# Optimization experiments

Measured on AMD Instinct MI355X. Metric: run time of the kernel, lower is better.

The kernel has to match this reference:

```python
import jax, jax.numpy as jnp
import numpy as np

E, D, H, T = 8, 1024, 2048, 2048  # num_expert, d_model, d_hidden, tokens

def setup_inputs() -> dict:
    key = jax.random.key(0)
    ks = jax.random.split(key, 7)
    return {
        "moe_inp": jax.random.normal(ks[0], (T, D), jnp.float32),
        "Wg": jax.random.normal(ks[1], (D, E), jnp.float32) * 0.02,
        "bg": jnp.zeros((E,), jnp.float32),
        "W1": jax.random.normal(ks[2], (E, D, H), jnp.float32) * 0.02,
        "b1": jnp.zeros((E, H), jnp.float32),
        "W2": jax.random.normal(ks[3], (E, H, D), jnp.float32) * 0.02,
        "b2": jnp.zeros((E, D), jnp.float32),
        "top_k": 2,
    }

def reference(moe_inp, Wg, bg, W1, b1, W2, b2, top_k):
    # NaiveGate: linear gate, top-k select, softmax over the selected logits
    logits = moe_inp @ Wg + bg                      # [T, E]
    top_vals, top_idx = jax.lax.top_k(logits, top_k)  # [T, k]
    gate_score = jax.nn.softmax(top_vals, axis=-1)    # [T, k]

    # Exact (no capacity drop) MoE: scan over experts, mask-combine.
    # Equivalent math to scatter -> per-expert FFN -> gather -> bmm(gate_score, ...).
    def body(acc, xs):
        e, w1, bb1, w2, bb2 = xs
        h = jax.nn.gelu(moe_inp @ w1 + bb1)          # [T, H]
        y = h @ w2 + bb2                             # [T, D]
        w = jnp.sum(jnp.where(top_idx == e, gate_score, 0.0), axis=-1)  # [T]
        return acc + w[:, None] * y, None

    init = jnp.zeros_like(moe_inp)
    xs = (jnp.arange(E), W1, b1, W2, b2)
    moe_outp, _ = jax.lax.scan(body, init, xs)
    return moe_outp, top_idx
```

## Files before the change

kernel.cpp:

```cpp
#include <hip/hip_runtime.h>
#include <stdint.h>

#define T_TOK 2048
#define D_DIM 1024
#define H_DIM 2048
#define N_EXP 8
#define MAXS  4608

#define WS_CNT    0
#define WS_BTOK   256
#define WS_BW     (WS_BTOK + N_EXP*2048*4)
#define WS_XG     (WS_BW + N_EXP*2048*4)
#define WS_HBUF   (WS_XG + (size_t)MAXS*1024*2)
#define WS_W1T    (WS_HBUF + (size_t)MAXS*2048*2)
#define WS_W2T    (WS_W1T + (size_t)N_EXP*1024*2048*2)

typedef __bf16 bf16x8 __attribute__((ext_vector_type(8)));
typedef float  f32x4  __attribute__((ext_vector_type(4)));

__device__ __forceinline__ unsigned short f2bf(float f) {
  unsigned int u = __float_as_uint(f);
  u += 0x7fffu + ((u >> 16) & 1u);
  return (unsigned short)(u >> 16);
}

__device__ __forceinline__ float gelu_tanh(float x) {
  const float u = 0.7978845608028654f * (x + 0.044715f * x * x * x);
  const float t = __expf(-2.0f * fabsf(u));
  const float th = (1.0f - t) * __builtin_amdgcn_rcpf(1.0f + t);
  return 0.5f * x * (1.0f + copysignf(th, u));
}

__global__ void zero_kernel(float4* __restrict__ out4, int* __restrict__ cnt) {
  int i = blockIdx.x * 256 + threadIdx.x;
  out4[i] = make_float4(0.f, 0.f, 0.f, 0.f);
  if (blockIdx.x == 0 && threadIdx.x < N_EXP) cnt[threadIdx.x] = 0;
}

__global__ void gate_kernel(const float* __restrict__ x, const float* __restrict__ Wg,
                            const float* __restrict__ bg, float* __restrict__ out_idx,
                            int* __restrict__ cnt, int* __restrict__ btok,
                            float* __restrict__ bw) {
  const int lane = threadIdx.x & 63;
  const int t = blockIdx.x * 4 + (threadIdx.x >> 6);
  float p[8];
#pragma unroll
  for (int i = 0; i < 8; ++i) p[i] = 0.f;
  const float* xr = x + (size_t)t * D_DIM;
  for (int i = lane; i < D_DIM; i += 64) {
    const float xv = xr[i];
    const float4 wa = ((const float4*)(Wg + i * 8))[0];
    const float4 wb = ((const float4*)(Wg + i * 8))[1];
    p[0] += xv * wa.x; p[1] += xv * wa.y; p[2] += xv * wa.z; p[3] += xv * wa.w;
    p[4] += xv * wb.x; p[5] += xv * wb.y; p[6] += xv * wb.z; p[7] += xv * wb.w;
  }
#pragma unroll
  for (int off = 32; off > 0; off >>= 1) {
#pragma unroll
    for (int i = 0; i < 8; ++i) p[i] += __shfl_xor(p[i], off);
  }
  if (lane == 0) {
#pragma unroll
    for (int i = 0; i < 8; ++i) p[i] += bg[i];
    int i0 = 0; float v0 = p[0];
#pragma unroll
    for (int i = 1; i < 8; ++i) if (p[i] > v0) { v0 = p[i]; i0 = i; }
    int i1 = -1; float v1 = -3.4e38f;
#pragma unroll
    for (int i = 0; i < 8; ++i) if (i != i0 && p[i] > v1) { v1 = p[i]; i1 = i; }
    const float ex = expf(v1 - v0);
    const float inv = 1.f / (1.f + ex);
    out_idx[t * 2 + 0] = (float)i0;
    out_idx[t * 2 + 1] = (float)i1;
    int s0 = atomicAdd(&cnt[i0], 1);
    btok[i0 * 2048 + s0] = t; bw[i0 * 2048 + s0] = inv;
    int s1 = atomicAdd(&cnt[i1], 1);
    btok[i1 * 2048 + s1] = t; bw[i1 * 2048 + s1] = ex * inv;
  }
}

__global__ void transpose_cvt(const float* __restrict__ W1, unsigned short* __restrict__ W1t,
                              const float* __restrict__ W2, unsigned short* __restrict__ W2t) {
  const int set = blockIdx.z;
  const int e = blockIdx.y;
  const int lin = blockIdx.x;
  const int R = set ? H_DIM : D_DIM;
  const int C = set ? D_DIM : H_DIM;
  const int tx = set ? (lin & 15) : (lin & 31);
  const int ty = set ? (lin >> 4) : (lin >> 5);
  const float* in = (set ? W2 : W1) + (size_t)e * (D_DIM * H_DIM);
  unsigned short* out = (set ? W2t : W1t) + (size_t)e * (D_DIM * H_DIM);
  const int c0 = tx * 64, r0 = ty * 64;
  __shared__ float tile[64][68];
  const int tid = threadIdx.x;
#pragma unroll
  for (int p = 0; p < 4; ++p) {
    const int idx = p * 256 + tid;
    const int r = idx >> 4, c4 = idx & 15;
    *(float4*)&tile[r][c4 * 4] = *(const float4*)(in + (size_t)(r0 + r) * C + c0 + c4 * 4);
  }
  __syncthreads();
#pragma unroll
  for (int p = 0; p < 2; ++p) {
    const int idx = p * 256 + tid;
    const int oc = idx >> 3, seg = idx & 7;
    unsigned u[4];
#pragma unroll
    for (int j = 0; j < 4; ++j) {
      const unsigned lo = f2bf(tile[seg * 8 + 2 * j][oc]);
      const unsigned hi = f2bf(tile[seg * 8 + 2 * j + 1][oc]);
      u[j] = lo | (hi << 16);
    }
    *(uint4*)(out + (size_t)(c0 + oc) * R + r0 + seg * 8) = make_uint4(u[0], u[1], u[2], u[3]);
  }
}

__device__ __forceinline__ void expert_seg(const int* __restrict__ cnt, int e,
                                           int& base, int& ce, int& pcnt, int& total) {
  int off = 0; base = 0; ce = 0; pcnt = 0;
#pragma unroll
  for (int i = 0; i < N_EXP; ++i) {
    const int c = cnt[i];
    const int p = (c + 63) & ~63;
    if (i == e) { base = off; ce = c; pcnt = p; }
    off += p;
  }
  total = off;
}

__global__ void gather_cvt(const float* __restrict__ x, const int* __restrict__ cnt,
                           const int* __restrict__ btok, unsigned short* __restrict__ Xg) {
  const int s = blockIdx.x;
  int off = 0, e = -1, loc = 0, c_e = 0;
#pragma unroll
  for (int i = 0; i < N_EXP; ++i) {
    const int c = cnt[i];
    const int p = (c + 63) & ~63;
    if (e < 0 && s < off + p) { e = i; loc = s - off; c_e = c; }
    off += p;
  }
  if (e < 0) return;
  uint2* orow = (uint2*)(Xg + (size_t)s * D_DIM);
  if (loc < c_e) {
    const int t = btok[e * 2048 + loc];
    const float4 v = ((const float4*)(x + (size_t)t * D_DIM))[threadIdx.x];
    uint2 u;
    u.x = (unsigned)f2bf(v.x) | ((unsigned)f2bf(v.y) << 16);
    u.y = (unsigned)f2bf(v.z) | ((unsigned)f2bf(v.w) << 16);
    orow[threadIdx.x] = u;
  } else {
    orow[threadIdx.x] = make_uint2(0u, 0u);
  }
}

template <int MODE>
__global__ void __launch_bounds__(256) moe_gemm(
    const unsigned short* __restrict__ A, const unsigned short* __restrict__ B,
    const float* __restrict__ bias, const int* __restrict__ cnt,
    const int* __restrict__ btok, const float* __restrict__ bw,
    unsigned short* __restrict__ Hout, float* __restrict__ out) {
  constexpr int K   = (MODE == 0) ? D_DIM : H_DIM;
  constexpr int SK  = (MODE == 0) ? 1 : 2;
  constexpr int KS  = K / SK;
  constexpr int NIT = KS / 32;

  const int lin = blockIdx.x;
  const int glo = lin & 7;
  const int mt  = (lin >> 3) & 31;
  const int g   = ((lin >> 8) << 3) | glo;
  int nt, e, ksl;
  if (MODE == 0) { nt = g & 15; e = g >> 4; ksl = 0; }
  else           { nt = g & 7;  e = (g >> 3) & 7; ksl = g >> 6; }

  int base, ce, pcnt, total;
  expert_seg(cnt, e, base, ce, pcnt, total);
  if (mt * 64 >= pcnt) return;
  const int row0 = base + mt * 64;
  const int n0 = nt * 128;

  __shared__ __align__(16) unsigned short As[2][64 * 32];
  __shared__ __align__(16) unsigned short Bs[2][128 * 32];

  const int tid = threadIdx.x;
  const int lane = tid & 63;
  const int wv = tid >> 6;
  const int wm = wv >> 1;
  const int wn = wv & 1;

  const unsigned short* Ab = A + (size_t)row0 * K + ksl * KS;
  const unsigned short* Bb = B + (size_t)e * ((size_t)H_DIM * D_DIM) + (size_t)n0 * K + ksl * KS;

  f32x4 acc[2][4];
#pragma unroll
  for (int i = 0; i < 2; ++i)
#pragma unroll
    for (int j = 0; j < 4; ++j) acc[i][j] = (f32x4)(0.0f);

  const int subr = lane >> 2;
  const int ks = (lane & 3) * 8;
  const int fr = lane & 15;
  const int kq = (lane >> 4) * 8;

  auto stage = [&](int kt, int b) {
    const int k0 = kt * 32;
    {
      const int r = wv * 16 + subr;
      const unsigned short* ga = Ab + (size_t)r * K + (k0 + ks);
      __builtin_amdgcn_global_load_lds(
          (__attribute__((address_space(1))) void*)ga,
          (__attribute__((address_space(3))) void*)(As[b] + wv * 16 * 32), 16, 0, 0);
    }
#pragma unroll
    for (int it = 0; it < 2; ++it) {
      const int ci = wv + it * 4;
      const int r = ci * 16 + subr;
      const unsigned short* gb = Bb + (size_t)r * K + (k0 + ks);
      __builtin_amdgcn_global_load_lds(
          (__attribute__((address_space(1))) void*)gb,
          (__attribute__((address_space(3))) void*)(Bs[b] + ci * 16 * 32), 16, 0, 0);
    }
  };

  stage(0, 0);
  for (int i = 0; i < NIT; ++i) {
    const int b = i & 1;
    __syncthreads();
    if (i + 1 < NIT) stage(i + 1, b ^ 1);
    bf16x8 av[2], bv[4];
#pragma unroll
    for (int mi = 0; mi < 2; ++mi)
      av[mi] = *(const bf16x8*)(As[b] + (wm * 32 + mi * 16 + fr) * 32 + kq);
#pragma unroll
    for (int ni = 0; ni < 4; ++ni)
      bv[ni] = *(const bf16x8*)(Bs[b] + (wn * 64 + ni * 16 + fr) * 32 + kq);
#pragma unroll
    for (int mi = 0; mi < 2; ++mi)
#pragma unroll
      for (int ni = 0; ni < 4; ++ni)
        acc[mi][ni] = __builtin_amdgcn_mfma_f32_16x16x32_bf16(av[mi], bv[ni], acc[mi][ni], 0, 0, 0);
  }

  if (MODE == 0) {
    const float* bb = bias + (size_t)e * H_DIM + n0;
#pragma unroll
    for (int mi = 0; mi < 2; ++mi) {
      const int rb = wm * 32 + mi * 16 + (lane >> 4) * 4;
#pragma unroll
      for (int r = 0; r < 4; ++r) {
        unsigned short* hp = Hout + (size_t)(row0 + rb + r) * H_DIM + n0;
#pragma unroll
        for (int ni = 0; ni < 4; ++ni) {
          const int col = wn * 64 + ni * 16 + fr;
          hp[col] = f2bf(gelu_tanh(acc[mi][ni][r] + bb[col]));
        }
      }
    }
  } else {
    const float* bb = bias + (size_t)e * D_DIM + n0;
#pragma unroll
    for (int mi = 0; mi < 2; ++mi) {
      const int rb = wm * 32 + mi * 16 + (lane >> 4) * 4;
#pragma unroll
      for (int r = 0; r < 4; ++r) {
        const int local = mt * 64 + rb + r;
        if (local < ce) {
          const int tok = btok[e * 2048 + local];
          const float w = bw[e * 2048 + local];
          float* op = out + (size_t)tok * D_DIM + n0;
#pragma unroll
          for (int ni = 0; ni < 4; ++ni) {
            const int col = wn * 64 + ni * 16 + fr;
            const float bias_once = (ksl == 0) ? bb[col] : 0.f;
            atomicAdd(op + col, w * (acc[mi][ni][r] + bias_once));
          }
        }
      }
    }
  }
}

extern "C" void kernel_launch(void* const* d_in, const int* in_sizes, int n_in,
                              void* d_out, int out_size, void* d_ws, size_t ws_size,
                              hipStream_t stream) {
  const float* moe_inp = (const float*)d_in[0];
  const float* Wg = (const float*)d_in[1];
  const float* bg = (const float*)d_in[2];
  const float* W1 = (const float*)d_in[3];
  const float* b1 = (const float*)d_in[4];
  const float* W2 = (const float*)d_in[5];
  const float* b2 = (const float*)d_in[6];
  float* out = (float*)d_out;

  char* ws = (char*)d_ws;
  int* cnt  = (int*)(ws + WS_CNT);
  int* btok = (int*)(ws + WS_BTOK);
  float* bw = (float*)(ws + WS_BW);
  unsigned short* Xg   = (unsigned short*)(ws + WS_XG);
  unsigned short* Hbuf = (unsigned short*)(ws + WS_HBUF);
  unsigned short* W1t  = (unsigned short*)(ws + WS_W1T);
  unsigned short* W2t  = (unsigned short*)(ws + WS_W2T);

  zero_kernel<<<dim3(2048), dim3(256), 0, stream>>>((float4*)out, cnt);
  gate_kernel<<<dim3(T_TOK / 4), dim3(256), 0, stream>>>(moe_inp, Wg, bg,
                                                         out + (size_t)T_TOK * D_DIM,
                                                         cnt, btok, bw);
  transpose_cvt<<<dim3(512, N_EXP, 2), dim3(256), 0, stream>>>(W1, W1t, W2, W2t);
  gather_cvt<<<dim3(MAXS), dim3(256), 0, stream>>>(moe_inp, cnt, btok, Xg);
  moe_gemm<0><<<dim3(4096), dim3(256), 0, stream>>>(
      Xg, W1t, b1, cnt, btok, bw, Hbuf, nullptr);
  moe_gemm<1><<<dim3(4096), dim3(256), 0, stream>>>(
      Hbuf, W2t, b2, cnt, btok, bw, nullptr, out);
}
```

Measured before the change: 333.2 us.

## Merge prep kernels and overlap W2 transpose with first expert GEMM

Zeroing, gating and the W1 transpose now run in one prep kernel, with the expert counters cleared by a memset. The W2 transpose blocks are appended to the first GEMM's grid so its bandwidth-bound work can overlap the compute-bound GEMM. This cuts kernel launches and lets idle CUs take transpose work during the first GEMM's tail. The trade-off is larger shared-memory allocations in the fused kernels, which may lower occupancy, and more branching on block index.

Result: faster. 318.5 us (-4.4%).

```diff
diff --git a/kernel.cpp b/kernel.cpp
--- a/kernel.cpp
+++ b/kernel.cpp
@@ -31,18 +31,43 @@
   return 0.5f * x * (1.0f + copysignf(th, u));
 }
 
-__global__ void zero_kernel(float4* __restrict__ out4, int* __restrict__ cnt) {
-  int i = blockIdx.x * 256 + threadIdx.x;
-  out4[i] = make_float4(0.f, 0.f, 0.f, 0.f);
-  if (blockIdx.x == 0 && threadIdx.x < N_EXP) cnt[threadIdx.x] = 0;
-}
-
-__global__ void gate_kernel(const float* __restrict__ x, const float* __restrict__ Wg,
-                            const float* __restrict__ bg, float* __restrict__ out_idx,
-                            int* __restrict__ cnt, int* __restrict__ btok,
-                            float* __restrict__ bw) {
+
+__device__ __forceinline__ void transpose_body(const float* __restrict__ in,
+                                               unsigned short* __restrict__ out,
+                                               int Rout, int Cin, int tx, int ty,
+                                               void* smem_) {
+  float (*tile)[68] = (float (*)[68])smem_;
+  const int c0 = tx * 64, r0 = ty * 64;
+  const int tid = threadIdx.x;
+#pragma unroll
+  for (int p = 0; p < 4; ++p) {
+    const int idx = p * 256 + tid;
+    const int r = idx >> 4, c4 = idx & 15;
+    *(float4*)&tile[r][c4 * 4] = *(const float4*)(in + (size_t)(r0 + r) * Cin + c0 + c4 * 4);
+  }
+  __syncthreads();
+#pragma unroll
+  for (int p = 0; p < 2; ++p) {
+    const int idx = p * 256 + tid;
+    const int oc = idx >> 3, seg = idx & 7;
+    unsigned u[4];
+#pragma unroll
+    for (int j = 0; j < 4; ++j) {
+      const unsigned lo = f2bf(tile[seg * 8 + 2 * j][oc]);
+      const unsigned hi = f2bf(tile[seg * 8 + 2 * j + 1][oc]);
+      u[j] = lo | (hi << 16);
+    }
+    *(uint4*)(out + (size_t)(c0 + oc) * Rout + r0 + seg * 8) = make_uint4(u[0], u[1], u[2], u[3]);
+  }
+}
+
+__device__ __forceinline__ void gate_body(int t, const float* __restrict__ x,
+                                          const float* __restrict__ Wg,
+                                          const float* __restrict__ bg,
+                                          float* __restrict__ out_idx,
+                                          int* __restrict__ cnt, int* __restrict__ btok,
+                                          float* __restrict__ bw) {
   const int lane = threadIdx.x & 63;
-  const int t = blockIdx.x * 4 + (threadIdx.x >> 6);
   float p[8];
 #pragma unroll
   for (int i = 0; i < 8; ++i) p[i] = 0.f;
@@ -79,42 +104,6 @@
   }
 }
 
-__global__ void transpose_cvt(const float* __restrict__ W1, unsigned short* __restrict__ W1t,
-                              const float* __restrict__ W2, unsigned short* __restrict__ W2t) {
-  const int set = blockIdx.z;
-  const int e = blockIdx.y;
-  const int lin = blockIdx.x;
-  const int R = set ? H_DIM : D_DIM;
-  const int C = set ? D_DIM : H_DIM;
-  const int tx = set ? (lin & 15) : (lin & 31);
-  const int ty = set ? (lin >> 4) : (lin >> 5);
-  const float* in = (set ? W2 : W1) + (size_t)e * (D_DIM * H_DIM);
-  unsigned short* out = (set ? W2t : W1t) + (size_t)e * (D_DIM * H_DIM);
-  const int c0 = tx * 64, r0 = ty * 64;
-  __shared__ float tile[64][68];
-  const int tid = threadIdx.x;
-#pragma unroll
-  for (int p = 0; p < 4; ++p) {
-    const int idx = p * 256 + tid;
-    const int r = idx >> 4, c4 = idx & 15;
-    *(float4*)&tile[r][c4 * 4] = *(const float4*)(in + (size_t)(r0 + r) * C + c0 + c4 * 4);
-  }
-  __syncthreads();
-#pragma unroll
-  for (int p = 0; p < 2; ++p) {
-    const int idx = p * 256 + tid;
-    const int oc = idx >> 3, seg = idx & 7;
-    unsigned u[4];
-#pragma unroll
-    for (int j = 0; j < 4; ++j) {
-      const unsigned lo = f2bf(tile[seg * 8 + 2 * j][oc]);
-      const unsigned hi = f2bf(tile[seg * 8 + 2 * j + 1][oc]);
-      u[j] = lo | (hi << 16);
-    }
-    *(uint4*)(out + (size_t)(c0 + oc) * R + r0 + seg * 8) = make_uint4(u[0], u[1], u[2], u[3]);
-  }
-}
-
 __device__ __forceinline__ void expert_seg(const int* __restrict__ cnt, int e,
                                            int& base, int& ce, int& pcnt, int& total) {
   int off = 0; base = 0; ce = 0; pcnt = 0;
@@ -126,6 +115,152 @@
     off += p;
   }
   total = off;
+}
+
+template <int MODE>
+__device__ __forceinline__ void gemm_body(
+    int lin, const unsigned short* __restrict__ A, const unsigned short* __restrict__ B,
+    const float* __restrict__ bias, const int* __restrict__ cnt,
+    const int* __restrict__ btok, const float* __restrict__ bw,
+    unsigned short* __restrict__ Hout, float* __restrict__ out, void* smem_) {
+  constexpr int K   = (MODE == 0) ? D_DIM : H_DIM;
+  constexpr int SK  = (MODE == 0) ? 1 : 2;
+  constexpr int KS  = K / SK;
+  constexpr int NIT = KS / 32;
+
+  const int glo = lin & 7;
+  const int mt  = (lin >> 3) & 31;
+  const int g   = ((lin >> 8) << 3) | glo;
+  int nt, e, ksl;
+  if (MODE == 0) { nt = g & 15; e = g >> 4; ksl = 0; }
+  else           { nt = g & 7;  e = (g >> 3) & 7; ksl = g >> 6; }
+
+  int base, ce, pcnt, total;
+  expert_seg(cnt, e, base, ce, pcnt, total);
+  if (mt * 64 >= pcnt) return;
+  const int row0 = base + mt * 64;
+  const int n0 = nt * 128;
+
+  unsigned short (*As)[64 * 32] = (unsigned short (*)[64 * 32])smem_;
+  unsigned short (*Bs)[128 * 32] = (unsigned short (*)[128 * 32])((char*)smem_ + 8192);
+
+  const int tid = threadIdx.x;
+  const int lane = tid & 63;
+  const int wv = tid >> 6;
+  const int wm = wv >> 1;
+  const int wn = wv & 1;
+
+  const unsigned short* Ab = A + (size_t)row0 * K + ksl * KS;
+  const unsigned short* Bb = B + (size_t)e * ((size_t)H_DIM * D_DIM) + (size_t)n0 * K + ksl * KS;
+
+  f32x4 acc[2][4];
+#pragma unroll
+  for (int i = 0; i < 2; ++i)
+#pragma unroll
+    for (int j = 0; j < 4; ++j) acc[i][j] = (f32x4)(0.0f);
+
+  const int subr = lane >> 2;
+  const int ks = (lane & 3) * 8;
+  const int fr = lane & 15;
+  const int kq = (lane >> 4) * 8;
+
+  auto stage = [&](int kt, int b) {
+    const int k0 = kt * 32;
+    {
+      const int r = wv * 16 + subr;
+      const unsigned short* ga = Ab + (size_t)r * K + (k0 + ks);
+      __builtin_amdgcn_global_load_lds(
+          (__attribute__((address_space(1))) void*)ga,
+          (__attribute__((address_space(3))) void*)(As[b] + wv * 16 * 32), 16, 0, 0);
+    }
+#pragma unroll
+    for (int it = 0; it < 2; ++it) {
+      const int ci = wv + it * 4;
+      const int r = ci * 16 + subr;
+      const unsigned short* gb = Bb + (size_t)r * K + (k0 + ks);
+      __builtin_amdgcn_global_load_lds(
+          (__attribute__((address_space(1))) void*)gb,
+          (__attribute__((address_space(3))) void*)(Bs[b] + ci * 16 * 32), 16, 0, 0);
+    }
+  };
+
+  stage(0, 0);
+  for (int i = 0; i < NIT; ++i) {
+    const int b = i & 1;
+    __syncthreads();
+    if (i + 1 < NIT) stage(i + 1, b ^ 1);
+    bf16x8 av[2], bv[4];
+#pragma unroll
+    for (int mi = 0; mi < 2; ++mi)
+      av[mi] = *(const bf16x8*)(As[b] + (wm * 32 + mi * 16 + fr) * 32 + kq);
+#pragma unroll
+    for (int ni = 0; ni < 4; ++ni)
+      bv[ni] = *(const bf16x8*)(Bs[b] + (wn * 64 + ni * 16 + fr) * 32 + kq);
+#pragma unroll
+    for (int mi = 0; mi < 2; ++mi)
+#pragma unroll
+      for (int ni = 0; ni < 4; ++ni)
+        acc[mi][ni] = __builtin_amdgcn_mfma_f32_16x16x32_bf16(av[mi], bv[ni], acc[mi][ni], 0, 0, 0);
+  }
+
+  if (MODE == 0) {
+    const float* bb = bias + (size_t)e * H_DIM + n0;
+#pragma unroll
+    for (int mi = 0; mi < 2; ++mi) {
+      const int rb = wm * 32 + mi * 16 + (lane >> 4) * 4;
+#pragma unroll
+      for (int r = 0; r < 4; ++r) {
+        unsigned short* hp = Hout + (size_t)(row0 + rb + r) * H_DIM + n0;
+#pragma unroll
+        for (int ni = 0; ni < 4; ++ni) {
+          const int col = wn * 64 + ni * 16 + fr;
+          hp[col] = f2bf(gelu_tanh(acc[mi][ni][r] + bb[col]));
+        }
+      }
+    }
+  } else {
+    const float* bb = bias + (size_t)e * D_DIM + n0;
+#pragma unroll
+    for (int mi = 0; mi < 2; ++mi) {
+      const int rb = wm * 32 + mi * 16 + (lane >> 4) * 4;
+#pragma unroll
+      for (int r = 0; r < 4; ++r) {
+        const int local = mt * 64 + rb + r;
+        if (local < ce) {
+          const int tok = btok[e * 2048 + local];
+          const float w = bw[e * 2048 + local];
+          float* op = out + (size_t)tok * D_DIM + n0;
+#pragma unroll
+          for (int ni = 0; ni < 4; ++ni) {
+            const int col = wn * 64 + ni * 16 + fr;
+            const float bias_once = (ksl == 0) ? bb[col] : 0.f;
+            atomicAdd(op + col, w * (acc[mi][ni][r] + bias_once));
+          }
+        }
+      }
+    }
+  }
+}
+
+
+__global__ void __launch_bounds__(256) prep_kernel(
+    const float* __restrict__ x, const float* __restrict__ Wg,
+    const float* __restrict__ bg, const float* __restrict__ W1,
+    float* __restrict__ out, int* __restrict__ cnt, int* __restrict__ btok,
+    float* __restrict__ bw, unsigned short* __restrict__ W1t) {
+  __shared__ __align__(16) char smem[17408];
+  const int bid = blockIdx.x;
+  if (bid < 2048) {
+    ((float4*)out)[bid * 256 + threadIdx.x] = make_float4(0.f, 0.f, 0.f, 0.f);
+  } else if (bid < 2560) {
+    gate_body((bid - 2048) * 4 + (threadIdx.x >> 6), x, Wg, bg,
+              out + (size_t)T_TOK * D_DIM, cnt, btok, bw);
+  } else {
+    const int lin = bid - 2560;
+    const int e = lin >> 9, l9 = lin & 511;
+    transpose_body(W1 + (size_t)e * (D_DIM * H_DIM), W1t + (size_t)e * (D_DIM * H_DIM),
+                   D_DIM, H_DIM, l9 & 31, l9 >> 5, smem);
+  }
 }
 
 __global__ void gather_cvt(const float* __restrict__ x, const int* __restrict__ cnt,
@@ -153,130 +288,30 @@
   }
 }
 
-template <int MODE>
-__global__ void __launch_bounds__(256) moe_gemm(
-    const unsigned short* __restrict__ A, const unsigned short* __restrict__ B,
-    const float* __restrict__ bias, const int* __restrict__ cnt,
+__global__ void __launch_bounds__(256) gemm0_w2t(
+    const unsigned short* __restrict__ Xg, const unsigned short* __restrict__ W1t,
+    const float* __restrict__ b1, const int* __restrict__ cnt,
     const int* __restrict__ btok, const float* __restrict__ bw,
-    unsigned short* __restrict__ Hout, float* __restrict__ out) {
-  constexpr int K   = (MODE == 0) ? D_DIM : H_DIM;
-  constexpr int SK  = (MODE == 0) ? 1 : 2;
-  constexpr int KS  = K / SK;
-  constexpr int NIT = KS / 32;
-
-  const int lin = blockIdx.x;
-  const int glo = lin & 7;
-  const int mt  = (lin >> 3) & 31;
-  const int g   = ((lin >> 8) << 3) | glo;
-  int nt, e, ksl;
-  if (MODE == 0) { nt = g & 15; e = g >> 4; ksl = 0; }
-  else           { nt = g & 7;  e = (g >> 3) & 7; ksl = g >> 6; }
-
-  int base, ce, pcnt, total;
-  expert_seg(cnt, e, base, ce, pcnt, total);
-  if (mt * 64 >= pcnt) return;
-  const int row0 = base + mt * 64;
-  const int n0 = nt * 128;
-
-  __shared__ __align__(16) unsigned short As[2][64 * 32];
-  __shared__ __align__(16) unsigned short Bs[2][128 * 32];
-
-  const int tid = threadIdx.x;
-  const int lane = tid & 63;
-  const int wv = tid >> 6;
-  const int wm = wv >> 1;
-  const int wn = wv & 1;
-
-  const unsigned short* Ab = A + (size_t)row0 * K + ksl * KS;
-  const unsigned short* Bb = B + (size_t)e * ((size_t)H_DIM * D_DIM) + (size_t)n0 * K + ksl * KS;
-
-  f32x4 acc[2][4];
-#pragma unroll
-  for (int i = 0; i < 2; ++i)
-#pragma unroll
-    for (int j = 0; j < 4; ++j) acc[i][j] = (f32x4)(0.0f);
-
-  const int subr = lane >> 2;
-  const int ks = (lane & 3) * 8;
-  const int fr = lane & 15;
-  const int kq = (lane >> 4) * 8;
-
-  auto stage = [&](int kt, int b) {
-    const int k0 = kt * 32;
-    {
-      const int r = wv * 16 + subr;
-      const unsigned short* ga = Ab + (size_t)r * K + (k0 + ks);
-      __builtin_amdgcn_global_load_lds(
-          (__attribute__((address_space(1))) void*)ga,
-          (__attribute__((address_space(3))) void*)(As[b] + wv * 16 * 32), 16, 0, 0);
-    }
-#pragma unroll
-    for (int it = 0; it < 2; ++it) {
-      const int ci = wv + it * 4;
-      const int r = ci * 16 + subr;
-      const unsigned short* gb = Bb + (size_t)r * K + (k0 + ks);
-      __builtin_amdgcn_global_load_lds(
-          (__attribute__((address_space(1))) void*)gb,
-          (__attribute__((address_space(3))) void*)(Bs[b] + ci * 16 * 32), 16, 0, 0);
-    }
-  };
-
-  stage(0, 0);
-  for (int i = 0; i < NIT; ++i) {
-    const int b = i & 1;
-    __syncthreads();
-    if (i + 1 < NIT) stage(i + 1, b ^ 1);
-    bf16x8 av[2], bv[4];
-#pragma unroll
-    for (int mi = 0; mi < 2; ++mi)
-      av[mi] = *(const bf16x8*)(As[b] + (wm * 32 + mi * 16 + fr) * 32 + kq);
-#pragma unroll
-    for (int ni = 0; ni < 4; ++ni)
-      bv[ni] = *(const bf16x8*)(Bs[b] + (wn * 64 + ni * 16 + fr) * 32 + kq);
-#pragma unroll
-    for (int mi = 0; mi < 2; ++mi)
-#pragma unroll
-      for (int ni = 0; ni < 4; ++ni)
-        acc[mi][ni] = __builtin_amdgcn_mfma_f32_16x16x32_bf16(av[mi], bv[ni], acc[mi][ni], 0, 0, 0);
-  }
-
-  if (MODE == 0) {
-    const float* bb = bias + (size_t)e * H_DIM + n0;
-#pragma unroll
-    for (int mi = 0; mi < 2; ++mi) {
-      const int rb = wm * 32 + mi * 16 + (lane >> 4) * 4;
-#pragma unroll
-      for (int r = 0; r < 4; ++r) {
-        unsigned short* hp = Hout + (size_t)(row0 + rb + r) * H_DIM + n0;
-#pragma unroll
-        for (int ni = 0; ni < 4; ++ni) {
-          const int col = wn * 64 + ni * 16 + fr;
-          hp[col] = f2bf(gelu_tanh(acc[mi][ni][r] + bb[col]));
-        }
-      }
-    }
+    unsigned short* __restrict__ Hbuf, const float* __restrict__ W2,
+    unsigned short* __restrict__ W2t) {
+  __shared__ __align__(16) char smem[24576];
+  if (blockIdx.x < 4096) {
+    gemm_body<0>(blockIdx.x, Xg, W1t, b1, cnt, btok, bw, Hbuf, nullptr, smem);
   } else {
-    const float* bb = bias + (size_t)e * D_DIM + n0;
-#pragma unroll
-    for (int mi = 0; mi < 2; ++mi) {
-      const int rb = wm * 32 + mi * 16 + (lane >> 4) * 4;
-#pragma unroll
-      for (int r = 0; r < 4; ++r) {
-        const int local = mt * 64 + rb + r;
-        if (local < ce) {
-          const int tok = btok[e * 2048 + local];
-          const float w = bw[e * 2048 + local];
-          float* op = out + (size_t)tok * D_DIM + n0;
-#pragma unroll
-          for (int ni = 0; ni < 4; ++ni) {
-            const int col = wn * 64 + ni * 16 + fr;
-            const float bias_once = (ksl == 0) ? bb[col] : 0.f;
-            atomicAdd(op + col, w * (acc[mi][ni][r] + bias_once));
-          }
-        }
-      }
-    }
-  }
+    const int lin = blockIdx.x - 4096;
+    const int e = lin >> 9, l9 = lin & 511;
+    transpose_body(W2 + (size_t)e * (D_DIM * H_DIM), W2t + (size_t)e * (D_DIM * H_DIM),
+                   H_DIM, D_DIM, l9 & 15, l9 >> 4, smem);
+  }
+}
+
+__global__ void __launch_bounds__(256) moe_gemm1(
+    const unsigned short* __restrict__ Hbuf, const unsigned short* __restrict__ W2t,
+    const float* __restrict__ b2, const int* __restrict__ cnt,
+    const int* __restrict__ btok, const float* __restrict__ bw,
+    float* __restrict__ out) {
+  __shared__ __align__(16) char smem[24576];
+  gemm_body<1>(blockIdx.x, Hbuf, W2t, b2, cnt, btok, bw, nullptr, out, smem);
 }
 
 extern "C" void kernel_launch(void* const* d_in, const int* in_sizes, int n_in,
@@ -300,14 +335,11 @@
   unsigned short* W1t  = (unsigned short*)(ws + WS_W1T);
   unsigned short* W2t  = (unsigned short*)(ws + WS_W2T);
 
-  zero_kernel<<<dim3(2048), dim3(256), 0, stream>>>((float4*)out, cnt);
-  gate_kernel<<<dim3(T_TOK / 4), dim3(256), 0, stream>>>(moe_inp, Wg, bg,
-                                                         out + (size_t)T_TOK * D_DIM,
-                                                         cnt, btok, bw);
-  transpose_cvt<<<dim3(512, N_EXP, 2), dim3(256), 0, stream>>>(W1, W1t, W2, W2t);
+  hipMemsetAsync(cnt, 0, 256, stream);
+  prep_kernel<<<dim3(6656), dim3(256), 0, stream>>>(moe_inp, Wg, bg, W1,
+                                                    out, cnt, btok, bw, W1t);
   gather_cvt<<<dim3(MAXS), dim3(256), 0, stream>>>(moe_inp, cnt, btok, Xg);
-  moe_gemm<0><<<dim3(4096), dim3(256), 0, stream>>>(
-      Xg, W1t, b1, cnt, btok, bw, Hbuf, nullptr);
-  moe_gemm<1><<<dim3(4096), dim3(256), 0, stream>>>(
-      Hbuf, W2t, b2, cnt, btok, bw, nullptr, out);
-}
+  gemm0_w2t<<<dim3(8192), dim3(256), 0, stream>>>(Xg, W1t, b1, cnt, btok, bw,
+                                                  Hbuf, W2, W2t);
+  moe_gemm1<<<dim3(4096), dim3(256), 0, stream>>>(Hbuf, W2t, b2, cnt, btok, bw, out);
+}
```
